# Kernel optimization log

Measured on AMD Instinct MI355X. Metric: run time of the kernel, lower is better.

The kernel has to match this reference:

```python
import jax, jax.numpy as jnp
import numpy as np


def conv1x1(x, W, b):
    # x: [B,C,H,W], W: [O,C], b: [O]  (torch Conv2d 1x1 squeezed)
    return jnp.einsum('oc,bchw->bohw', W, x) + b[None, :, None, None]


def setup_inputs() -> dict:
    key = jax.random.key(0)
    ks = jax.random.split(key, 7)
    B, C, H, W = 8, 256, 32, 32
    s = 1.0 / np.sqrt(C)
    x = jax.random.normal(ks[0], (B, C, H, W), jnp.float32)
    Wq = jax.random.normal(ks[1], (C, C), jnp.float32) * s
    bq = jax.random.normal(ks[2], (C,), jnp.float32) * 0.01
    Wk = jax.random.normal(ks[3], (C, C), jnp.float32) * s
    bk = jax.random.normal(ks[4], (C,), jnp.float32) * 0.01
    Wo = jax.random.normal(ks[5], (C, C), jnp.float32) * s
    bo = jax.random.normal(ks[6], (C,), jnp.float32) * 0.01
    return {"x": x, "Wq": Wq, "bq": bq, "Wk": Wk, "bk": bk, "Wo": Wo, "bo": bo}


def reference(x, Wq, bq, Wk, bk, Wo, bo):
    B, C, H, W = x.shape
    HW = H * W
    scale = 1.0 / (C ** 0.5)
    # proj_query: torch does view(B,C,HW).permute(0,2,1).transpose(1,2).contiguous().view(-1,C)
    # which is a row-major reshape of [B,C,HW] into [B*HW, C] (channel/spatial interleaved).
    # Reproduced faithfully.
    q = conv1x1(x, Wq, bq).reshape(B, C, HW).reshape(-1, C)          # [B*HW, C]
    # proj_key: view(B,C,HW).transpose(0,1).contiguous().view(C,-1) -> true [C, B*HW]
    k = jnp.transpose(conv1x1(x, Wk, bk).reshape(B, C, HW), (1, 0, 2)).reshape(C, -1)
    x_w = (q @ k).reshape(B * HW, B, HW)                              # [BHW, B, HW]
    out_co = jnp.max(x_w, axis=-1) + jnp.mean(x_w, axis=-1)           # [BHW, B]
    x_co = jnp.mean(out_co, axis=-1).reshape(B, HW) * scale           # [B, HW]
    x_co = jax.nn.softmax(x_co, axis=-1).reshape(B, 1, H, W)
    return conv1x1(x * x_co, Wo, bo)
```

## Files before the change

kernel.cpp:

```cpp
#include <hip/hip_runtime.h>

#define BATCH 8
#define CH 256
#define HWSZ 1024
#define BHW 8192

typedef _Float16 f16;
typedef _Float16 f16x4 __attribute__((ext_vector_type(4)));
typedef _Float16 f16x8 __attribute__((ext_vector_type(8)));
typedef float f32x4 __attribute__((ext_vector_type(4)));
typedef unsigned long long u64;
typedef __attribute__((address_space(3))) unsigned int lds_u32;
typedef __attribute__((address_space(1))) const unsigned int glob_u32;

__global__ __launch_bounds__(256) void kmeanW_kernel(
    const float* __restrict__ Wk, const float* __restrict__ bk,
    const float* __restrict__ xsum, float* __restrict__ kmean)
{
    __shared__ float xm[CH];
    const int b = blockIdx.x;
    const int tid = threadIdx.x;
    xm[tid] = xsum[b * 256 + tid] * (1.0f / HWSZ);
    __syncthreads();

    float acc = 0.f;
    const float4* w = (const float4*)(Wk + tid * CH);
    for (int c4 = 0; c4 < 64; ++c4) {
        float4 wv = w[c4];
        acc = fmaf(wv.x, xm[c4 * 4 + 0], acc);
        acc = fmaf(wv.y, xm[c4 * 4 + 1], acc);
        acc = fmaf(wv.z, xm[c4 * 4 + 2], acc);
        acc = fmaf(wv.w, xm[c4 * 4 + 3], acc);
    }
    kmean[b * 256 + tid] = acc + bk[tid];
}

__global__ __launch_bounds__(512, 1) void pgemmQKY_kernel(
    const float* __restrict__ x,
    const float* __restrict__ Wq, const float* __restrict__ Wk, const float* __restrict__ Wo,
    const float* __restrict__ bq, const float* __restrict__ bk,
    f16* __restrict__ Qh, char* __restrict__ Ksw, f16* __restrict__ Yh,
    float* __restrict__ xsum)
{
    __shared__ __align__(16) char kbuf[32 * 1024];
    __shared__ __align__(16) float xt[256][36];
    f16* tile = (f16*)&xt[0][0];
    char* tileb = (char*)&xt[0][0];

    const int pxg0 = blockIdx.x * 32;
    const int b    = pxg0 >> 10;
    const int hw0  = pxg0 & 1023;
    const int tid  = threadIdx.x;
    const int lane = tid & 63;
    const int wid  = tid >> 6;
    const int m = lane & 15, g = lane >> 4;

    {
        const int f4 = tid & 7;
        const int cs = tid >> 3;
#pragma unroll
        for (int pass = 0; pass < 4; ++pass) {
            const int c = pass * 64 + cs;
            float4 v = *(const float4*)(x + ((size_t)b * CH + c) * HWSZ + hw0 + f4 * 4);
            *(float4*)&xt[c][f4 * 4] = v;
        }
    }
    __syncthreads();

    {
        const int px = tid & 31;
        const int q8 = tid >> 5;
        const int sw = (px & 7) << 4;
#pragma unroll
        for (int r = 0; r < 2; ++r) {
            f16x8 hi, lo;
#pragma unroll
            for (int i = 0; i < 8; ++i) {
                const int c = q8 * 16 + r * 8 + i;
                float v = xt[c][px];
                f16 h = (f16)v;
                hi[i] = h;
                lo[i] = (f16)(v - (float)h);
            }
            const int base = q8 * 32 + r * 16;
            *(f16x8*)(kbuf + px * 1024 + (base ^ sw)) = hi;
            *(f16x8*)(kbuf + px * 1024 + 512 + (base ^ sw)) = lo;
        }
    }

    if (tid < 256) {
        float s = 0.f;
#pragma unroll
        for (int i4 = 0; i4 < 8; ++i4) {
            float4 v = *(const float4*)&xt[tid][i4 * 4];
            s += v.x + v.y + v.z + v.w;
        }
        atomicAdd(&xsum[b * 256 + tid], s);
    }

    f16x8 aA[2][8], aB[2][8];
#define LOAD_W(dst, Wsel)                                                                \
    {                                                                                    \
        _Pragma("unroll")                                                                \
        for (int t = 0; t < 2; ++t)                                                      \
            _Pragma("unroll")                                                            \
            for (int kk = 0; kk < 8; ++kk) {                                             \
                const float* wrow = (Wsel) + (size_t)(wid * 32 + t * 16 + m) * CH + kk * 32 + g * 8; \
                float4 w0 = *(const float4*)(wrow);                                      \
                float4 w1 = *(const float4*)(wrow + 4);                                  \
                f16x8 av;                                                                \
                av[0] = (f16)w0.x; av[1] = (f16)w0.y; av[2] = (f16)w0.z; av[3] = (f16)w0.w; \
                av[4] = (f16)w1.x; av[5] = (f16)w1.y; av[6] = (f16)w1.z; av[7] = (f16)w1.w; \
                dst[t][kk] = av;                                                         \
            }                                                                            \
    }
    LOAD_W(aA, Wq);
    __syncthreads();

    const int sw0 = (m & 7) << 4;
    const f32x4 vz = {0.f, 0.f, 0.f, 0.f};
    f32x4 acc[2][2];

#define MFMA_PASS(ARR, NKS)                                                              \
    {                                                                                    \
        _Pragma("unroll")                                                                \
        for (int t = 0; t < 2; ++t) { acc[t][0] = vz; acc[t][1] = vz; }                  \
        _Pragma("unroll")                                                                \
        for (int ks = 0; ks < (NKS); ++ks) {                                             \
            const int X = ks * 64 + g * 16;                                              \
            f16x8 b0 = *(const f16x8*)(kbuf + m * 1024 + (X ^ sw0));                     \
            f16x8 b1 = *(const f16x8*)(kbuf + (16 + m) * 1024 + (X ^ sw0));              \
            _Pragma("unroll")                                                            \
            for (int t = 0; t < 2; ++t) {                                                \
                acc[t][0] = __builtin_amdgcn_mfma_f32_16x16x32_f16(ARR[t][ks & 7], b0, acc[t][0], 0, 0, 0); \
                acc[t][1] = __builtin_amdgcn_mfma_f32_16x16x32_f16(ARR[t][ks & 7], b1, acc[t][1], 0, 0, 0); \
            }                                                                            \
        }                                                                                \
    }

    MFMA_PASS(aA, 16);
    LOAD_W(aB, Wk);

#pragma unroll
    for (int t = 0; t < 2; ++t) {
        const int co0 = wid * 32 + t * 16 + 4 * g;
        float4 bv = *(const float4*)(bq + co0);
        float ba[4] = {bv.x, bv.y, bv.z, bv.w};
#pragma unroll
        for (int u = 0; u < 2; ++u) {
            const int px = u * 16 + m;
#pragma unroll
            for (int j = 0; j < 4; ++j)
                tile[(co0 + j) * 32 + (px ^ (j << 3))] = (f16)(acc[t][u][j] + ba[j]);
        }
    }
    __syncthreads();
#pragma unroll
    for (int pass = 0; pass < 2; ++pass) {
        const int co  = pass * 128 + (tid >> 2);
        const int run = tid & 3;
        f16x8 v = *(const f16x8*)(tile + co * 32 + ((run * 8) ^ ((co & 3) << 3)));
        *(f16x8*)(Qh + ((size_t)b * CH + co) * HWSZ + hw0 + run * 8) = v;
    }

    MFMA_PASS(aB, 16);
    LOAD_W(aA, Wo);
    __syncthreads();

#pragma unroll
    for (int t = 0; t < 2; ++t) {
        const int co0 = wid * 32 + t * 16 + 4 * g;
        float4 bv = *(const float4*)(bk + co0);
        float ba[4] = {bv.x, bv.y, bv.z, bv.w};
#pragma unroll
        for (int u = 0; u < 2; ++u) {
            const int px = u * 16 + m;
            f16x4 pk;
#pragma unroll
            for (int j = 0; j < 4; ++j) pk[j] = (f16)(acc[t][u][j] + ba[j]);
            *(f16x4*)(tileb + px * 512 + ((co0 * 2) ^ (m << 3))) = pk;
        }
    }
    __syncthreads();
    {
        const int px = tid & 31;
        const int rp = tid >> 5;
        const int kloc = (px & 15) << 3;
        const int kglb = (px & 7) << 4;
        char* grow = Ksw + (size_t)(pxg0 + px) * 512;
#pragma unroll
        for (int i = 0; i < 2; ++i) {
            const int r = rp + i * 16;
            u64 a0 = *(const u64*)(tileb + px * 512 + ((r * 16) ^ kloc));
            u64 a1 = *(const u64*)(tileb + px * 512 + ((r * 16 + 8) ^ kloc));
            char* gdst = grow + ((r * 16) ^ kglb);
            *(u64*)gdst = a0;
            *(u64*)(gdst + 8) = a1;
        }
    }

    MFMA_PASS(aA, 8);
    __syncthreads();

#pragma unroll
    for (int t = 0; t < 2; ++t) {
        const int co0 = wid * 32 + t * 16 + 4 * g;
#pragma unroll
        for (int u = 0; u < 2; ++u) {
            const int px = u * 16 + m;
#pragma unroll
            for (int j = 0; j < 4; ++j)
                tile[(co0 + j) * 32 + (px ^ (j << 3))] = (f16)acc[t][u][j];
        }
    }
    __syncthreads();
#pragma unroll
    for (int pass = 0; pass < 2; ++pass) {
        const int co  = pass * 128 + (tid >> 2);
        const int run = tid & 3;
        f16x8 v = *(const f16x8*)(tile + co * 32 + ((run * 8) ^ ((co & 3) << 3)));
        *(f16x8*)(Yh + ((size_t)b * CH + co) * HWSZ + hw0 + run * 8) = v;
    }
#undef MFMA_PASS
#undef LOAD_W
}

__global__ __launch_bounds__(256, 2) void score_kernel(
    const f16* __restrict__ Qh, const char* __restrict__ Ksw,
    const float* __restrict__ kmean, float* __restrict__ logits)
{
    __shared__ __align__(16) char kbuf[2][32768];
    __shared__ float lds_rm[128][2];
    __shared__ float lds_dq[128];
    __shared__ float km[CH];

    const int batch = blockIdx.x & 7;
    const int r0    = (blockIdx.x >> 3) * 128;
    const int tid   = threadIdx.x;
    const int lane  = tid & 63;
    const int wid   = tid >> 6;
    const int wr = wid >> 1, wc = wid & 1;
    const int m = lane & 15, g = lane >> 4;
    const int rbase = r0 + wr * 64;

    km[tid] = kmean[batch * 256 + tid];

    const char* kbase = Ksw + (size_t)batch * HWSZ * 512;

#define STAGE(buf, ch)                                                                   \
    {                                                                                    \
        const char* _src = kbase + (ch) * 64 * 512 + tid * 16;                           \
        char* _dst = &kbuf[buf][tid * 16];                                               \
        _Pragma("unroll")                                                                \
        for (int k = 0; k < 8; ++k)                                                      \
            __builtin_amdgcn_global_load_lds((glob_u32*)(_src + k * 4096),               \
                                             (lds_u32*)(_dst + k * 4096), 16, 0, 0);     \
    }

    STAGE(0, 0);

    f16x8 a[4][8];
#pragma unroll
    for (int t = 0; t < 4; ++t)
#pragma unroll
        for (int kk = 0; kk < 8; ++kk)
            a[t][kk] = *(const f16x8*)(Qh + (size_t)(rbase + t * 16 + m) * CH + kk * 32 + 8 * g);

    int boff[8][2];
    {
        const int sw = (m & 7) << 4;
#pragma unroll
        for (int kk = 0; kk < 8; ++kk)
#pragma unroll
            for (int u2 = 0; u2 < 2; ++u2) {
                const int col = wc * 32 + u2 * 16 + m;
                boff[kk][u2] = col * 512 + ((kk * 64 + g * 16) ^ sw);
            }
    }

    float rm[4][4];
#pragma unroll
    for (int t = 0; t < 4; ++t)
#pragma unroll
        for (int jj = 0; jj < 4; ++jj) rm[t][jj] = -1e30f;

    int cur = 0;
    for (int ch = 0; ch < 16; ++ch) {
        if (ch < 15) {
            STAGE(cur ^ 1, ch + 1);
            asm volatile("s_waitcnt vmcnt(8)" ::: "memory");
        } else {
            asm volatile("s_waitcnt vmcnt(0)" ::: "memory");
        }
        __builtin_amdgcn_s_barrier();

        const char* kb = &kbuf[cur][0];
        f32x4 acc[4][2];
        const f32x4 vz = {0.f, 0.f, 0.f, 0.f};
#pragma unroll
        for (int t = 0; t < 4; ++t) { acc[t][0] = vz; acc[t][1] = vz; }

#pragma unroll
        for (int kk = 0; kk < 8; ++kk) {
            f16x8 bfr[2];
            bfr[0] = *(const f16x8*)(kb + boff[kk][0]);
            bfr[1] = *(const f16x8*)(kb + boff[kk][1]);
#pragma unroll
            for (int t = 0; t < 4; ++t) {
                acc[t][0] = __builtin_amdgcn_mfma_f32_16x16x32_f16(a[t][kk], bfr[0], acc[t][0], 0, 0, 0);
                acc[t][1] = __builtin_amdgcn_mfma_f32_16x16x32_f16(a[t][kk], bfr[1], acc[t][1], 0, 0, 0);
            }
        }

#pragma unroll
        for (int t = 0; t < 4; ++t)
#pragma unroll
            for (int jj = 0; jj < 4; ++jj)
                rm[t][jj] = fmaxf(rm[t][jj], fmaxf(acc[t][0][jj], acc[t][1][jj]));

        asm volatile("" ::: "memory");
        __builtin_amdgcn_s_barrier();
        cur ^= 1;
    }
#undef STAGE

#pragma unroll
    for (int d = 1; d < 16; d <<= 1)
#pragma unroll
        for (int t = 0; t < 4; ++t)
#pragma unroll
            for (int jj = 0; jj < 4; ++jj)
                rm[t][jj] = fmaxf(rm[t][jj], __shfl_xor(rm[t][jj], d, 64));

    float dq[4];
#pragma unroll
    for (int t = 0; t < 4; ++t) {
        float s = 0.f;
#pragma unroll
        for (int kk = 0; kk < 8; ++kk)
#pragma unroll
            for (int i = 0; i < 8; ++i)
                s = fmaf((float)a[t][kk][i], km[kk * 32 + 8 * g + i], s);
        s += __shfl_xor(s, 16, 64);
        s += __shfl_xor(s, 32, 64);
        dq[t] = s;
    }

    if (m == 0) {
#pragma unroll
        for (int t = 0; t < 4; ++t)
#pragma unroll
            for (int jj = 0; jj < 4; ++jj)
                lds_rm[wr * 64 + t * 16 + g * 4 + jj][wc] = rm[t][jj];
    }
    if (wc == 0 && lane < 16) {
#pragma unroll
        for (int t = 0; t < 4; ++t)
            lds_dq[wr * 64 + t * 16 + lane] = dq[t];
    }
    __syncthreads();
    if (tid < 128) {
        float v = fmaxf(lds_rm[tid][0], lds_rm[tid][1]) + lds_dq[tid];
        atomicAdd(logits + r0 + tid, v * (1.0f / 128.0f));
    }
}

__global__ __launch_bounds__(256) void softmax_kernel(const float* __restrict__ logits,
                                                      float* __restrict__ wgt)
{
    const int br = blockIdx.x, tid = threadIdx.x;
    __shared__ float red[256];
    float l[4];
#pragma unroll
    for (int i = 0; i < 4; ++i) l[i] = logits[br * HWSZ + i * 256 + tid];

    float mx = fmaxf(fmaxf(l[0], l[1]), fmaxf(l[2], l[3]));
    red[tid] = mx;
    __syncthreads();
    for (int s = 128; s > 0; s >>= 1) {
        if (tid < s) red[tid] = fmaxf(red[tid], red[tid + s]);
        __syncthreads();
    }
    mx = red[0];
    __syncthreads();

    float e[4], sm = 0.f;
#pragma unroll
    for (int i = 0; i < 4; ++i) { e[i] = expf(l[i] - mx); sm += e[i]; }
    red[tid] = sm;
    __syncthreads();
    for (int s = 128; s > 0; s >>= 1) {
        if (tid < s) red[tid] += red[tid + s];
        __syncthreads();
    }
    const float inv = 1.0f / red[0];
#pragma unroll
    for (int i = 0; i < 4; ++i)
        wgt[br * HWSZ + i * 256 + tid] = e[i] * inv;
}

__global__ __launch_bounds__(256) void gateY_kernel(const f16* __restrict__ Yh,
                                                    const float* __restrict__ wgt,
                                                    const float* __restrict__ bo,
                                                    float* __restrict__ out)
{
    const size_t idx = ((size_t)blockIdx.x * 256 + threadIdx.x) * 8;
    const int b  = (int)(idx >> 18);
    const int c  = (int)(idx >> 10) & 255;
    const int hw = (int)idx & 1023;

    f16x8 y = *(const f16x8*)(Yh + idx);
    float4 w0 = *(const float4*)(wgt + b * HWSZ + hw);
    float4 w1 = *(const float4*)(wgt + b * HWSZ + hw + 4);
    const float bov = bo[c];

    float4 o0, o1;
    o0.x = fmaf((float)y[0], w0.x, bov); o0.y = fmaf((float)y[1], w0.y, bov);
    o0.z = fmaf((float)y[2], w0.z, bov); o0.w = fmaf((float)y[3], w0.w, bov);
    o1.x = fmaf((float)y[4], w1.x, bov); o1.y = fmaf((float)y[5], w1.y, bov);
    o1.z = fmaf((float)y[6], w1.z, bov); o1.w = fmaf((float)y[7], w1.w, bov);
    *(float4*)(out + idx)     = o0;
    *(float4*)(out + idx + 4) = o1;
}

extern "C" void kernel_launch(void* const* d_in, const int* in_sizes, int n_in,
                              void* d_out, int out_size, void* d_ws, size_t ws_size,
                              hipStream_t stream)
{
    const float* x  = (const float*)d_in[0];
    const float* Wq = (const float*)d_in[1];
    const float* bq = (const float*)d_in[2];
    const float* Wk = (const float*)d_in[3];
    const float* bk = (const float*)d_in[4];
    const float* Wo = (const float*)d_in[5];
    const float* bo = (const float*)d_in[6];
    float* out = (float*)d_out;

    char* ws = (char*)d_ws;
    f16*   Qh     = (f16*)(ws);
    char*  Ksw    = (char*)(ws + (4 << 20));
    f16*   Yh     = (f16*)(ws + (8 << 20));
    float* xsum   = (float*)(ws + (12 << 20));
    float* logits = (float*)(ws + (12 << 20) + (8 << 10));
    float* kmean  = (float*)(ws + (12 << 20) + (40 << 10));
    float* wgt    = (float*)(ws + (12 << 20) + (48 << 10));

    hipMemsetAsync(xsum, 0, 40 << 10, stream);

    pgemmQKY_kernel<<<dim3(256),  512, 0, stream>>>(x, Wq, Wk, Wo, bq, bk, Qh, Ksw, Yh, xsum);
    kmeanW_kernel  <<<dim3(8),    256, 0, stream>>>(Wk, bk, xsum, kmean);
    score_kernel   <<<dim3(512),  256, 0, stream>>>(Qh, Ksw, kmean, logits);
    softmax_kernel <<<dim3(8),    256, 0, stream>>>(logits, wgt);
    gateY_kernel   <<<dim3(1024), 256, 0, stream>>>(Yh, wgt, bo, out);
}
```

Baseline: 91.34 us.

## Split projection GEMM over output-channel halves and replace logit atomics with per-batch partials

The QKY projection kernel now launches 512 blocks of 256 threads, each computing 128 output channels for a 32-pixel tile. This doubles the grid and lets two blocks share a CU, at the cost of each block reloading and converting its x tile. The score kernel writes per-batch row partials to a buffer instead of atomically adding into logits; the softmax kernel sums the eight partials, which removes atomic contention and shrinks the memset. The kmean kernel is re-parallelised so each block covers 32 output channels across all batches instead of one batch per block.

```diff
diff --git a/kernel.cpp b/kernel.cpp
--- a/kernel.cpp
+++ b/kernel.cpp
@@ -17,25 +17,27 @@
     const float* __restrict__ Wk, const float* __restrict__ bk,
     const float* __restrict__ xsum, float* __restrict__ kmean)
 {
-    __shared__ float xm[CH];
-    const int b = blockIdx.x;
+    __shared__ float xm[BATCH][CH];
     const int tid = threadIdx.x;
-    xm[tid] = xsum[b * 256 + tid] * (1.0f / HWSZ);
-    __syncthreads();
-
+#pragma unroll
+    for (int i = 0; i < 8; ++i) xm[i][tid] = xsum[i * 256 + tid] * (1.0f / HWSZ);
+    __syncthreads();
+
+    const int co = blockIdx.x * 32 + (tid >> 3);
+    const int b  = tid & 7;
     float acc = 0.f;
-    const float4* w = (const float4*)(Wk + tid * CH);
+    const float4* w = (const float4*)(Wk + (size_t)co * CH);
     for (int c4 = 0; c4 < 64; ++c4) {
         float4 wv = w[c4];
-        acc = fmaf(wv.x, xm[c4 * 4 + 0], acc);
-        acc = fmaf(wv.y, xm[c4 * 4 + 1], acc);
-        acc = fmaf(wv.z, xm[c4 * 4 + 2], acc);
-        acc = fmaf(wv.w, xm[c4 * 4 + 3], acc);
-    }
-    kmean[b * 256 + tid] = acc + bk[tid];
-}
-
-__global__ __launch_bounds__(512, 1) void pgemmQKY_kernel(
+        acc = fmaf(wv.x, xm[b][c4 * 4 + 0], acc);
+        acc = fmaf(wv.y, xm[b][c4 * 4 + 1], acc);
+        acc = fmaf(wv.z, xm[b][c4 * 4 + 2], acc);
+        acc = fmaf(wv.w, xm[b][c4 * 4 + 3], acc);
+    }
+    kmean[b * 256 + co] = acc + bk[co];
+}
+
+__global__ __launch_bounds__(256, 2) void pgemmQKY_kernel(
     const float* __restrict__ x,
     const float* __restrict__ Wq, const float* __restrict__ Wk, const float* __restrict__ Wo,
     const float* __restrict__ bq, const float* __restrict__ bk,
@@ -47,20 +49,24 @@
     f16* tile = (f16*)&xt[0][0];
     char* tileb = (char*)&xt[0][0];
 
-    const int pxg0 = blockIdx.x * 32;
+    const int bid  = blockIdx.x;
+    const int h    = bid >> 8;
+    const int p    = bid & 255;
+    const int pxg0 = p * 32;
     const int b    = pxg0 >> 10;
     const int hw0  = pxg0 & 1023;
     const int tid  = threadIdx.x;
     const int lane = tid & 63;
     const int wid  = tid >> 6;
     const int m = lane & 15, g = lane >> 4;
+    const int coW = h * 128;
 
     {
         const int f4 = tid & 7;
         const int cs = tid >> 3;
 #pragma unroll
-        for (int pass = 0; pass < 4; ++pass) {
-            const int c = pass * 64 + cs;
+        for (int pass = 0; pass < 8; ++pass) {
+            const int c = pass * 32 + cs;
             float4 v = *(const float4*)(x + ((size_t)b * CH + c) * HWSZ + hw0 + f4 * 4);
             *(float4*)&xt[c][f4 * 4] = v;
         }
@@ -72,23 +78,23 @@
         const int q8 = tid >> 5;
         const int sw = (px & 7) << 4;
 #pragma unroll
-        for (int r = 0; r < 2; ++r) {
+        for (int r = 0; r < 4; ++r) {
             f16x8 hi, lo;
 #pragma unroll
             for (int i = 0; i < 8; ++i) {
-                const int c = q8 * 16 + r * 8 + i;
+                const int c = q8 * 32 + r * 8 + i;
                 float v = xt[c][px];
-                f16 h = (f16)v;
-                hi[i] = h;
-                lo[i] = (f16)(v - (float)h);
+                f16 hv = (f16)v;
+                hi[i] = hv;
+                lo[i] = (f16)(v - (float)hv);
             }
-            const int base = q8 * 32 + r * 16;
+            const int base = q8 * 64 + r * 16;
             *(f16x8*)(kbuf + px * 1024 + (base ^ sw)) = hi;
             *(f16x8*)(kbuf + px * 1024 + 512 + (base ^ sw)) = lo;
         }
     }
 
-    if (tid < 256) {
+    if (h == 0) {
         float s = 0.f;
 #pragma unroll
         for (int i4 = 0; i4 < 8; ++i4) {
@@ -98,30 +104,30 @@
         atomicAdd(&xsum[b * 256 + tid], s);
     }
 
-    f16x8 aA[2][8], aB[2][8];
-#define LOAD_W(dst, Wsel)                                                                \
+    f16x8 a[2][8];
+#define LOAD_W(Wsel)                                                                     \
     {                                                                                    \
         _Pragma("unroll")                                                                \
         for (int t = 0; t < 2; ++t)                                                      \
             _Pragma("unroll")                                                            \
             for (int kk = 0; kk < 8; ++kk) {                                             \
-                const float* wrow = (Wsel) + (size_t)(wid * 32 + t * 16 + m) * CH + kk * 32 + g * 8; \
+                const float* wrow = (Wsel) + (size_t)(coW + wid * 32 + t * 16 + m) * CH + kk * 32 + g * 8; \
                 float4 w0 = *(const float4*)(wrow);                                      \
                 float4 w1 = *(const float4*)(wrow + 4);                                  \
                 f16x8 av;                                                                \
                 av[0] = (f16)w0.x; av[1] = (f16)w0.y; av[2] = (f16)w0.z; av[3] = (f16)w0.w; \
                 av[4] = (f16)w1.x; av[5] = (f16)w1.y; av[6] = (f16)w1.z; av[7] = (f16)w1.w; \
-                dst[t][kk] = av;                                                         \
+                a[t][kk] = av;                                                           \
             }                                                                            \
     }
-    LOAD_W(aA, Wq);
+    LOAD_W(Wq);
     __syncthreads();
 
     const int sw0 = (m & 7) << 4;
     const f32x4 vz = {0.f, 0.f, 0.f, 0.f};
     f32x4 acc[2][2];
 
-#define MFMA_PASS(ARR, NKS)                                                              \
+#define MFMA_PASS(NKS)                                                                   \
     {                                                                                    \
         _Pragma("unroll")                                                                \
         for (int t = 0; t < 2; ++t) { acc[t][0] = vz; acc[t][1] = vz; }                  \
@@ -132,45 +138,44 @@
             f16x8 b1 = *(const f16x8*)(kbuf + (16 + m) * 1024 + (X ^ sw0));              \
             _Pragma("unroll")                                                            \
             for (int t = 0; t < 2; ++t) {                                                \
-                acc[t][0] = __builtin_amdgcn_mfma_f32_16x16x32_f16(ARR[t][ks & 7], b0, acc[t][0], 0, 0, 0); \
-                acc[t][1] = __builtin_amdgcn_mfma_f32_16x16x32_f16(ARR[t][ks & 7], b1, acc[t][1], 0, 0, 0); \
+                acc[t][0] = __builtin_amdgcn_mfma_f32_16x16x32_f16(a[t][ks & 7], b0, acc[t][0], 0, 0, 0); \
+                acc[t][1] = __builtin_amdgcn_mfma_f32_16x16x32_f16(a[t][ks & 7], b1, acc[t][1], 0, 0, 0); \
             }                                                                            \
         }                                                                                \
     }
 
-    MFMA_PASS(aA, 16);
-    LOAD_W(aB, Wk);
+    MFMA_PASS(16);
 
 #pragma unroll
     for (int t = 0; t < 2; ++t) {
-        const int co0 = wid * 32 + t * 16 + 4 * g;
-        float4 bv = *(const float4*)(bq + co0);
+        const int lco0 = wid * 32 + t * 16 + 4 * g;
+        float4 bv = *(const float4*)(bq + coW + lco0);
         float ba[4] = {bv.x, bv.y, bv.z, bv.w};
 #pragma unroll
         for (int u = 0; u < 2; ++u) {
             const int px = u * 16 + m;
 #pragma unroll
             for (int j = 0; j < 4; ++j)
-                tile[(co0 + j) * 32 + (px ^ (j << 3))] = (f16)(acc[t][u][j] + ba[j]);
+                tile[(lco0 + j) * 32 + (px ^ (j << 3))] = (f16)(acc[t][u][j] + ba[j]);
         }
     }
     __syncthreads();
 #pragma unroll
     for (int pass = 0; pass < 2; ++pass) {
-        const int co  = pass * 128 + (tid >> 2);
+        const int lco = pass * 64 + (tid >> 2);
         const int run = tid & 3;
-        f16x8 v = *(const f16x8*)(tile + co * 32 + ((run * 8) ^ ((co & 3) << 3)));
-        *(f16x8*)(Qh + ((size_t)b * CH + co) * HWSZ + hw0 + run * 8) = v;
-    }
-
-    MFMA_PASS(aB, 16);
-    LOAD_W(aA, Wo);
+        f16x8 v = *(const f16x8*)(tile + lco * 32 + ((run * 8) ^ ((lco & 3) << 3)));
+        *(f16x8*)(Qh + ((size_t)b * CH + coW + lco) * HWSZ + hw0 + run * 8) = v;
+    }
+
+    LOAD_W(Wk);
+    MFMA_PASS(16);
     __syncthreads();
 
 #pragma unroll
     for (int t = 0; t < 2; ++t) {
-        const int co0 = wid * 32 + t * 16 + 4 * g;
-        float4 bv = *(const float4*)(bk + co0);
+        const int lco0 = wid * 32 + t * 16 + 4 * g;
+        float4 bv = *(const float4*)(bk + coW + lco0);
         float ba[4] = {bv.x, bv.y, bv.z, bv.w};
 #pragma unroll
         for (int u = 0; u < 2; ++u) {
@@ -178,7 +183,7 @@
             f16x4 pk;
 #pragma unroll
             for (int j = 0; j < 4; ++j) pk[j] = (f16)(acc[t][u][j] + ba[j]);
-            *(f16x4*)(tileb + px * 512 + ((co0 * 2) ^ (m << 3))) = pk;
+            *(f16x4*)(tileb + px * 256 + ((lco0 * 2) ^ (m << 3))) = pk;
         }
     }
     __syncthreads();
@@ -187,39 +192,40 @@
         const int rp = tid >> 5;
         const int kloc = (px & 15) << 3;
         const int kglb = (px & 7) << 4;
-        char* grow = Ksw + (size_t)(pxg0 + px) * 512;
+        char* grow = Ksw + (size_t)(pxg0 + px) * 512 + h * 256;
 #pragma unroll
         for (int i = 0; i < 2; ++i) {
-            const int r = rp + i * 16;
-            u64 a0 = *(const u64*)(tileb + px * 512 + ((r * 16) ^ kloc));
-            u64 a1 = *(const u64*)(tileb + px * 512 + ((r * 16 + 8) ^ kloc));
-            char* gdst = grow + ((r * 16) ^ kglb);
+            const int rl = rp + i * 8;
+            u64 a0 = *(const u64*)(tileb + px * 256 + ((rl * 16) ^ kloc));
+            u64 a1 = *(const u64*)(tileb + px * 256 + ((rl * 16 + 8) ^ kloc));
+            char* gdst = grow + ((rl * 16) ^ kglb);
             *(u64*)gdst = a0;
             *(u64*)(gdst + 8) = a1;
         }
     }
 
-    MFMA_PASS(aA, 8);
+    LOAD_W(Wo);
+    MFMA_PASS(8);
     __syncthreads();
 
 #pragma unroll
     for (int t = 0; t < 2; ++t) {
-        const int co0 = wid * 32 + t * 16 + 4 * g;
+        const int lco0 = wid * 32 + t * 16 + 4 * g;
 #pragma unroll
         for (int u = 0; u < 2; ++u) {
             const int px = u * 16 + m;
 #pragma unroll
             for (int j = 0; j < 4; ++j)
-                tile[(co0 + j) * 32 + (px ^ (j << 3))] = (f16)acc[t][u][j];
+                tile[(lco0 + j) * 32 + (px ^ (j << 3))] = (f16)acc[t][u][j];
         }
     }
     __syncthreads();
 #pragma unroll
     for (int pass = 0; pass < 2; ++pass) {
-        const int co  = pass * 128 + (tid >> 2);
+        const int lco = pass * 64 + (tid >> 2);
         const int run = tid & 3;
-        f16x8 v = *(const f16x8*)(tile + co * 32 + ((run * 8) ^ ((co & 3) << 3)));
-        *(f16x8*)(Yh + ((size_t)b * CH + co) * HWSZ + hw0 + run * 8) = v;
+        f16x8 v = *(const f16x8*)(tile + lco * 32 + ((run * 8) ^ ((lco & 3) << 3)));
+        *(f16x8*)(Yh + ((size_t)b * CH + coW + lco) * HWSZ + hw0 + run * 8) = v;
     }
 #undef MFMA_PASS
 #undef LOAD_W
@@ -227,7 +233,7 @@
 
 __global__ __launch_bounds__(256, 2) void score_kernel(
     const f16* __restrict__ Qh, const char* __restrict__ Ksw,
-    const float* __restrict__ kmean, float* __restrict__ logits)
+    const float* __restrict__ kmean, float* __restrict__ rowdq)
 {
     __shared__ __align__(16) char kbuf[2][32768];
     __shared__ float lds_rm[128][2];
@@ -359,20 +365,24 @@
             lds_dq[wr * 64 + t * 16 + lane] = dq[t];
     }
     __syncthreads();
-    if (tid < 128) {
-        float v = fmaxf(lds_rm[tid][0], lds_rm[tid][1]) + lds_dq[tid];
-        atomicAdd(logits + r0 + tid, v * (1.0f / 128.0f));
-    }
-}
-
-__global__ __launch_bounds__(256) void softmax_kernel(const float* __restrict__ logits,
+    if (tid < 128)
+        rowdq[(size_t)(r0 + tid) * 8 + batch] =
+            fmaxf(lds_rm[tid][0], lds_rm[tid][1]) + lds_dq[tid];
+}
+
+__global__ __launch_bounds__(256) void softmax_kernel(const float* __restrict__ rowdq,
                                                       float* __restrict__ wgt)
 {
     const int br = blockIdx.x, tid = threadIdx.x;
     __shared__ float red[256];
     float l[4];
 #pragma unroll
-    for (int i = 0; i < 4; ++i) l[i] = logits[br * HWSZ + i * 256 + tid];
+    for (int i = 0; i < 4; ++i) {
+        const size_t r = (size_t)br * HWSZ + i * 256 + tid;
+        float4 v0 = *(const float4*)(rowdq + r * 8);
+        float4 v1 = *(const float4*)(rowdq + r * 8 + 4);
+        l[i] = (v0.x + v0.y + v0.z + v0.w + v1.x + v1.y + v1.z + v1.w) * (1.0f / 128.0f);
+    }
 
     float mx = fmaxf(fmaxf(l[0], l[1]), fmaxf(l[2], l[3]));
     red[tid] = mx;
@@ -441,15 +451,15 @@
     char*  Ksw    = (char*)(ws + (4 << 20));
     f16*   Yh     = (f16*)(ws + (8 << 20));
     float* xsum   = (float*)(ws + (12 << 20));
-    float* logits = (float*)(ws + (12 << 20) + (8 << 10));
-    float* kmean  = (float*)(ws + (12 << 20) + (40 << 10));
-    float* wgt    = (float*)(ws + (12 << 20) + (48 << 10));
-
-    hipMemsetAsync(xsum, 0, 40 << 10, stream);
-
-    pgemmQKY_kernel<<<dim3(256),  512, 0, stream>>>(x, Wq, Wk, Wo, bq, bk, Qh, Ksw, Yh, xsum);
+    float* rowdq  = (float*)(ws + (12 << 20) + (8 << 10));
+    float* kmean  = (float*)(ws + (12 << 20) + (264 << 10));
+    float* wgt    = (float*)(ws + (12 << 20) + (272 << 10));
+
+    hipMemsetAsync(xsum, 0, 8 << 10, stream);
+
+    pgemmQKY_kernel<<<dim3(512),  256, 0, stream>>>(x, Wq, Wk, Wo, bq, bk, Qh, Ksw, Yh, xsum);
     kmeanW_kernel  <<<dim3(8),    256, 0, stream>>>(Wk, bk, xsum, kmean);
-    score_kernel   <<<dim3(512),  256, 0, stream>>>(Qh, Ksw, kmean, logits);
-    softmax_kernel <<<dim3(8),    256, 0, stream>>>(logits, wgt);
+    score_kernel   <<<dim3(512),  256, 0, stream>>>(Qh, Ksw, kmean, rowdq);
+    softmax_kernel <<<dim3(8),    256, 0, stream>>>(rowdq, wgt);
     gateY_kernel   <<<dim3(1024), 256, 0, stream>>>(Yh, wgt, bo, out);
 }
```

After: 88.71 us. 1.03x faster.
